# Optimization experiments

Measured on AMD Instinct MI355X. Metric: run time of the kernel, lower is better.

The kernel has to match this reference:

```python
import math
import jax, jax.numpy as jnp
import numpy as np
from jax import lax

CELL_SIZE = 8
N_BINS = 9
SIGNED = False


def _conv3x3(x, k):
    # x: [N,1,H,W], k: [1,1,3,3]; padding=1 (SAME), stride 1
    return lax.conv_general_dilated(
        x, k, window_strides=(1, 1), padding=[(1, 1), (1, 1)],
        dimension_numbers=("NCHW", "OIHW", "NCHW"))


def setup_inputs() -> dict:
    key = jax.random.key(0)
    x = jax.random.uniform(key, (64, 1, 512, 512), dtype=jnp.float32)
    sobel_x = jnp.array([[-1., 0., 1.], [-2., 0., 2.], [-1., 0., 1.]],
                        dtype=jnp.float32).reshape(1, 1, 3, 3)
    sobel_y = jnp.array([[-1., -2., -1.], [0., 0., 0.], [1., 2., 1.]],
                        dtype=jnp.float32).reshape(1, 1, 3, 3)
    return {"x": x, "sobel_x": sobel_x, "sobel_y": sobel_y}


def reference(x, sobel_x, sobel_y):
    n, _, H, W = x.shape
    angle_range = 2 * math.pi if SIGNED else math.pi

    gx = _conv3x3(x, sobel_x)  # [N,1,H,W]
    gy = _conv3x3(x, sobel_y)
    mag = jnp.sqrt(gx * gx + gy * gy)          # [N,1,H,W]
    ang = jnp.arctan2(gx, gy)                  # note: atan2(gx, gy) as in source
    ang = ang + math.pi if SIGNED else jnp.abs(ang)
    bins = jnp.floor(ang / angle_range * (N_BINS - 1)).astype(jnp.int32)  # [N,1,H,W]

    # scatter_(dim=1): one-hot write of magnitudes into bin channel
    onehot = jax.nn.one_hot(bins[:, 0], N_BINS, axis=1, dtype=mag.dtype)  # [N,nb,H,W]
    out = onehot * mag                                                     # [N,nb,H,W]

    # AvgPool2d(cell,stride=cell) * cell**2 == sum over each cell
    cs = CELL_SIZE
    hog = out.reshape(n, N_BINS, H // cs, cs, W // cs, cs).sum(axis=(3, 5))
    return hog.reshape(-1)
```

## Files before the change

### kernel.cpp

```cpp
#include <hip/hip_runtime.h>
#include <math.h>

#define IMG_H 512
#define IMG_W 512
#define NB 9

__global__ __launch_bounds__(256, 4) void hog_kernel(const float* __restrict__ x,
                                                     float* __restrict__ out) {
#pragma clang fp contract(off)
    const int tid  = threadIdx.x;
    const int w    = tid >> 6;
    const int lane = tid & 63;
    const int cl   = lane & 15;
    const int qid  = lane >> 4;
    const int sr   = qid >> 1;
    const int sc   = qid & 1;

    const int cx = (w << 4) | cl;
    const int cy = blockIdx.x;
    const int n  = blockIdx.y;

    const float* img = x + (size_t)n * (IMG_H * IMG_W);
    const int x0 = (cx << 3) + (sc << 2);
    const int y0 = (cy << 3) + (sr << 2);

    float r[6][6];
#pragma unroll
    for (int i = 0; i < 6; ++i) {
        const int y = y0 - 1 + i;
        if (y < 0 || y >= IMG_H) {
#pragma unroll
            for (int j = 0; j < 6; ++j) r[i][j] = 0.0f;
        } else {
            const float* row = img + (size_t)y * IMG_W;
            const float4 p = *(const float4*)(row + x0);
            r[i][1] = p.x; r[i][2] = p.y; r[i][3] = p.z; r[i][4] = p.w;
            r[i][0] = (x0 == 0)           ? 0.0f : row[x0 - 1];
            r[i][5] = (x0 + 4 >= IMG_W)   ? 0.0f : row[x0 + 4];
        }
    }

    float accP[4], accN[4], acc8;
#pragma unroll
    for (int k = 0; k < 4; ++k) { accP[k] = 0.0f; accN[k] = 0.0f; }
    acc8 = 0.0f;

    const float PI_F = 3.14159274101257324f;
    const float T1F  = 0.41421356237309503f;
    const float T3F  = 2.41421356237309503f;
    const float KPI  = 2.54647909f;
    const float EPS  = 5e-5f;

    unsigned msk = 0u;

#pragma unroll
    for (int ry = 0; ry < 4; ++ry) {
#pragma unroll
        for (int j = 0; j < 4; ++j) {
            const float A0 = r[ry][j],     A1 = r[ry][j + 1], A2 = r[ry][j + 2];
            const float B0 = r[ry + 1][j],                    B2 = r[ry + 1][j + 2];
            const float C0 = r[ry + 2][j], C1 = r[ry + 2][j + 1], C2 = r[ry + 2][j + 2];

            const float gx = ((-A0 + (A2 - 2.0f * B0)) + (2.0f * B2 - C0)) + C2;
            const float gy = (((-A0 - 2.0f * A1) + (-A2)) + (C0 + 2.0f * C1)) + C2;

            const float u = fabsf(gx);
            const float W = fabsf(gy);
            const float q = u * u + W * W;
            const float mag = __builtin_amdgcn_sqrtf(q);

            const float b1 = W * T1F;
            const float b3 = W * T3F;
            const bool c1 = u > b1;
            const bool c2 = u > W;
            const bool c3 = u > b3;
            const bool s  = gy > 0.0f;

            const float KW = KPI * W;
            const float E  = EPS * q;
            const float md = fminf(fminf(fabsf(u - b1), fabsf(u - b3)),
                                   fminf(fabsf(u - W), u));
            const bool flag = md * KW < E;
            msk |= flag ? (1u << (ry * 4 + j)) : 0u;

            const float w0 = flag ? 0.0f : mag;
            const float wP = s ? w0 : 0.0f;
            const float wN = w0 - wP;
            accP[0] += wP;
            accP[1] += c1 ? wP : 0.0f;
            accP[2] += c2 ? wP : 0.0f;
            accP[3] += c3 ? wP : 0.0f;
            accN[0] += wN;
            accN[1] += c1 ? wN : 0.0f;
            accN[2] += c2 ? wN : 0.0f;
            accN[3] += c3 ? wN : 0.0f;
        }
    }

    if (msk) {
        auto add_bin = [&](int b, float v) {
            accP[0] += (b <= 3)           ? v : 0.0f;
            accP[1] += (b >= 1 && b <= 3) ? v : 0.0f;
            accP[2] += (b >= 2 && b <= 3) ? v : 0.0f;
            accP[3] += (b == 3)           ? v : 0.0f;
            accN[0] += (b >= 4 && b <= 7) ? v : 0.0f;
            accN[1] += (b >= 4 && b <= 6) ? v : 0.0f;
            accN[2] += (b >= 4 && b <= 5) ? v : 0.0f;
            accN[3] += (b == 4)           ? v : 0.0f;
            acc8    += (b == 8)           ? v : 0.0f;
        };
#pragma unroll
        for (int ry = 0; ry < 4; ++ry) {
#pragma unroll
            for (int j = 0; j < 4; ++j) {
                if (msk & (1u << (ry * 4 + j))) {
                    const float A0 = r[ry][j],     A1 = r[ry][j + 1], A2 = r[ry][j + 2];
                    const float B0 = r[ry + 1][j],                    B2 = r[ry + 1][j + 2];
                    const float C0 = r[ry + 2][j], C1 = r[ry + 2][j + 1], C2 = r[ry + 2][j + 2];
                    const float gx = ((-A0 + (A2 - 2.0f * B0)) + (2.0f * B2 - C0)) + C2;
                    const float gy = (((-A0 - 2.0f * A1) + (-A2)) + (C0 + 2.0f * C1)) + C2;
                    const float u = fabsf(gx);
                    const float W = fabsf(gy);
                    const float q = u * u + W * W;
                    const float mag = __builtin_amdgcn_sqrtf(q);

                    const float angf = (float)atan2((double)u, (double)gy);
                    const float tc = (float)((double)angf / (double)PI_F) * 8.0f;
                    int bc = (int)tc;
                    int bin = bc > 8 ? 8 : bc;
                    float wA = mag;
                    const float tn = roundf(tc);
                    const int B = (int)tn;
                    if (B >= 1 && B <= 8 && fabsf(tc - tn) < 4e-6f &&
                        mag <= 1.05f) {
                        const float hw = 0.5f * mag;
                        add_bin(B, hw);
                        bin = B - 1; wA = hw;
                    }
                    add_bin(bin, wA);
                }
            }
        }
    }

    const float vals[NB] = {accP[0] - accP[1], accP[1] - accP[2],
                            accP[2] - accP[3], accP[3],
                            accN[3],           accN[2] - accN[3],
                            accN[1] - accN[2], accN[0] - accN[1], acc8};
    float red[NB];
#pragma unroll
    for (int k = 0; k < NB; ++k) {
        float v = vals[k];
        v += __int_as_float(
                 __builtin_amdgcn_ds_swizzle(__float_as_int(v), 0x401F));
        v += __shfl_xor(v, 32, 64);
        red[k] = v;
    }

    const float v0 = qid == 0 ? red[0] : qid == 1 ? red[1]
                   : qid == 2 ? red[2] : red[3];
    const float v1 = qid == 0 ? red[4] : qid == 1 ? red[5]
                   : qid == 2 ? red[6] : red[7];
    float* o = out + (size_t)n * (NB * 64 * 64) + (size_t)cy * 64 + cx;
    o[(size_t)qid * 4096] = v0;
    o[(size_t)(qid + 4) * 4096] = v1;
    if (qid == 0) o[(size_t)8 * 4096] = red[8];
}

extern "C" void kernel_launch(void* const* d_in, const int* in_sizes, int n_in,
                              void* d_out, int out_size, void* d_ws, size_t ws_size,
                              hipStream_t stream) {
    const float* x = (const float*)d_in[0];
    float* out = (float*)d_out;
    hog_kernel<<<dim3(64, 64, 1), dim3(256, 1, 1), 0, stream>>>(x, out);
}
```

Baseline: 113.1 us.

## Remap lanes so quadrants are adjacent and fetch halo columns via cross-lane shuffles

Lanes are remapped so the four quadrant threads of a cell are consecutive lanes, which makes each wave's float4 row loads cover contiguous 32-byte spans per cell. The scalar halo column loads are replaced with shfl_xor and ds_bpermute exchanges from neighbouring lanes, and only wave-edge lanes still load from global memory. The final reduction becomes two xor shuffles over adjacent lanes. This trades two uncoalesced scalar global loads per row for several LDS-crossbar permutes per row, and it alters the output store pattern.

```diff
diff --git a/kernel.cpp b/kernel.cpp
--- a/kernel.cpp
+++ b/kernel.cpp
@@ -11,8 +11,8 @@
     const int tid  = threadIdx.x;
     const int w    = tid >> 6;
     const int lane = tid & 63;
-    const int cl   = lane & 15;
-    const int qid  = lane >> 4;
+    const int qid  = lane & 3;
+    const int cl   = lane >> 2;
     const int sr   = qid >> 1;
     const int sc   = qid & 1;
 
@@ -24,20 +24,36 @@
     const int x0 = (cx << 3) + (sc << 2);
     const int y0 = (cy << 3) + (sr << 2);
 
+    const int baddr = ((lane + (sc ? 3 : -3)) & 63) << 2;
+    const bool inAvail = sc ? (cl < 15) : (cl > 0);
+    const int ocol = sc ? x0 + 4 : x0 - 1;
+    const bool oLoad = !inAvail && (ocol >= 0) && (ocol < IMG_W);
+
     float r[6][6];
 #pragma unroll
     for (int i = 0; i < 6; ++i) {
         const int y = y0 - 1 + i;
-        if (y < 0 || y >= IMG_H) {
-#pragma unroll
-            for (int j = 0; j < 6; ++j) r[i][j] = 0.0f;
-        } else {
-            const float* row = img + (size_t)y * IMG_W;
-            const float4 p = *(const float4*)(row + x0);
-            r[i][1] = p.x; r[i][2] = p.y; r[i][3] = p.z; r[i][4] = p.w;
-            r[i][0] = (x0 == 0)           ? 0.0f : row[x0 - 1];
-            r[i][5] = (x0 + 4 >= IMG_W)   ? 0.0f : row[x0 + 4];
-        }
+        const bool vy = (y >= 0) && (y < IMG_H);
+        const float* row = img + (size_t)(vy ? y : 0) * IMG_W;
+        const float4 p = *(const float4*)(row + x0);
+
+        const float in_pw = __shfl_xor(p.w, 1, 64);
+        const float in_px = __shfl_xor(p.x, 1, 64);
+
+        const float expose = sc ? p.w : p.x;
+        const float outv = __int_as_float(
+            __builtin_amdgcn_ds_bpermute(baddr, __float_as_int(expose)));
+
+        float oval = 0.0f;
+        if (oLoad) oval = row[ocol];
+        const float outer = inAvail ? outv : oval;
+
+        r[i][1] = vy ? p.x : 0.0f;
+        r[i][2] = vy ? p.y : 0.0f;
+        r[i][3] = vy ? p.z : 0.0f;
+        r[i][4] = vy ? p.w : 0.0f;
+        r[i][0] = vy ? (sc ? in_pw : outer) : 0.0f;
+        r[i][5] = vy ? (sc ? outer : in_px) : 0.0f;
     }
 
     float accP[4], accN[4], acc8;
@@ -151,9 +167,8 @@
 #pragma unroll
     for (int k = 0; k < NB; ++k) {
         float v = vals[k];
-        v += __int_as_float(
-                 __builtin_amdgcn_ds_swizzle(__float_as_int(v), 0x401F));
-        v += __shfl_xor(v, 32, 64);
+        v += __shfl_xor(v, 1, 64);
+        v += __shfl_xor(v, 2, 64);
         red[k] = v;
     }
 
```

Result: no change. 114.7 us (+1.4%).
